# Kernel tuning notes

Hardware: AMD Instinct MI355X
Metric: run time of the kernel (lower is better)

The kernel has to match this reference:

```python
import jax, jax.numpy as jnp
import numpy as np

NUM_HEADS = 32


def setup_inputs() -> dict:
    key = jax.random.key(0)
    ks = jax.random.split(key, 6)
    B, S, D = 1, 2048, 4096
    hd = D // NUM_HEADS  # 128
    x = jax.random.normal(ks[0], (B, S, D), dtype=jnp.float32)
    # true rotary frequencies: freqs_cis = exp(i * t * theta^{-2j/hd})
    inv_freq = 1.0 / (10000.0 ** (jnp.arange(0, hd, 2, dtype=jnp.float32) / hd))  # [hd//2]
    angles = jnp.arange(S, dtype=jnp.float32)[:, None] * inv_freq[None, :]  # [S, hd//2]
    freqs_cos = jnp.cos(angles)
    freqs_sin = jnp.sin(angles)
    scale = 0.02
    wq = jax.random.normal(ks[1], (D, D), dtype=jnp.float32) * scale
    wk = jax.random.normal(ks[2], (D, D), dtype=jnp.float32) * scale
    wv = jax.random.normal(ks[3], (D, D), dtype=jnp.float32) * scale
    wo = jax.random.normal(ks[4], (D, D), dtype=jnp.float32) * scale
    return {"x": x, "freqs_cos": freqs_cos, "freqs_sin": freqs_sin,
            "wq": wq, "wk": wk, "wv": wv, "wo": wo}


def _apply_rope(t, cos, sin):
    # t: [B, S, H, hd]; cos/sin: [S, hd//2]
    B, S, H, hd = t.shape
    tr = t.reshape(B, S, H, hd // 2, 2)
    a, b = tr[..., 0], tr[..., 1]
    c = cos[None, :, None, :]
    s = sin[None, :, None, :]
    out_r = a * c - b * s
    out_i = a * s + b * c
    return jnp.stack([out_r, out_i], axis=-1).reshape(B, S, H, hd)


def reference(x, freqs_cos, freqs_sin, wq, wk, wv, wo):
    B, S, D = x.shape
    H = NUM_HEADS
    hd = D // H
    xq = (x @ wq).reshape(B, S, H, hd)
    xk = (x @ wk).reshape(B, S, H, hd)
    xv = (x @ wv).reshape(B, S, H, hd)
    xq = _apply_rope(xq, freqs_cos, freqs_sin)
    xk = _apply_rope(xk, freqs_cos, freqs_sin)
    # [B, H, S, hd]
    xq = xq.transpose(0, 2, 1, 3)
    xk = xk.transpose(0, 2, 1, 3)
    xv = xv.transpose(0, 2, 1, 3)
    scores = jnp.einsum('bhqd,bhkd->bhqk', xq, xk) / jnp.sqrt(jnp.float32(hd))
    scores = jax.nn.softmax(scores.astype(jnp.float32), axis=-1).astype(xq.dtype)
    out = jnp.einsum('bhqk,bhkd->bhqd', scores, xv)
    out = out.transpose(0, 2, 1, 3).reshape(B, S, D)
    return out @ wo
```

## Files before the change

### kernel.cpp

```cpp
#include <hip/hip_runtime.h>
#include <hip/hip_bf16.h>

typedef __hip_bfloat16 bf16;
typedef __attribute__((ext_vector_type(8))) short short8;
typedef __attribute__((ext_vector_type(4))) short short4v;
typedef __attribute__((ext_vector_type(4))) float f32x4;

#define MFMA16(a, b, c) __builtin_amdgcn_mfma_f32_16x16x32_bf16((a), (b), (c), 0, 0, 0)
#define EXP2(x) __builtin_amdgcn_exp2f(x)

static __device__ __forceinline__ void gload_lds16(const bf16* g, bf16* l) {
  __builtin_amdgcn_global_load_lds((const __attribute__((address_space(1))) unsigned int*)g,
                                   (__attribute__((address_space(3))) unsigned int*)l,
                                   16, 0, 0);
}

__global__ __launch_bounds__(256) void prepN_kernel(const float* __restrict__ x,
                                                    bf16* __restrict__ xb,
                                                    const float* __restrict__ wq,
                                                    const float* __restrict__ wk,
                                                    const float* __restrict__ wv,
                                                    const float* __restrict__ wo,
                                                    bf16* __restrict__ wT2,
                                                    bf16* __restrict__ wvT,
                                                    bf16* __restrict__ woT) {
  int y = blockIdx.y;
  if (y == 2) {
    int i = (blockIdx.x * 256 + threadIdx.x) * 8;
    float4 v0 = *(const float4*)(x + i);
    float4 v1 = *(const float4*)(x + i + 4);
    bf16 tmp[8];
    tmp[0] = __float2bfloat16(v0.x); tmp[1] = __float2bfloat16(v0.y);
    tmp[2] = __float2bfloat16(v0.z); tmp[3] = __float2bfloat16(v0.w);
    tmp[4] = __float2bfloat16(v1.x); tmp[5] = __float2bfloat16(v1.y);
    tmp[6] = __float2bfloat16(v1.z); tmp[7] = __float2bfloat16(v1.w);
    *(short8*)(xb + i) = *(short8*)tmp;
    return;
  }
  const float* W;
  bf16* WT;
  if (y == 0)      { W = wq; WT = wT2; }
  else if (y == 1) { W = wk; WT = wT2 + (size_t)4096 * 4096; }
  else if (y == 3) { W = wv; WT = wvT; }
  else             { W = wo; WT = woT; }
  __shared__ bf16 tile[64][65];
  int b = blockIdx.x;
  int tk = (b >> 6) * 64;
  int tn = (b & 63) * 64;
  int t = threadIdx.x;
  int c = t & 63, r0 = t >> 6;
#pragma unroll
  for (int i = 0; i < 16; ++i) {
    int r = i * 4 + r0;
    tile[c][r] = __float2bfloat16(W[(size_t)(tk + r) * 4096 + tn + c]);
  }
  __syncthreads();
#pragma unroll
  for (int i = 0; i < 16; ++i) {
    int r = i * 4 + r0;
    WT[(size_t)(tn + r) * 4096 + tk + c] = tile[r][c];
  }
}

__global__ __launch_bounds__(256) void tw_kernel(const float* __restrict__ W,
                                                 bf16* __restrict__ WT) {
  __shared__ bf16 tile[64][65];
  int b = blockIdx.x;
  int tk = (b >> 6) * 64;
  int tn = (b & 63) * 64;
  int t = threadIdx.x;
  int c = t & 63, r0 = t >> 6;
#pragma unroll
  for (int i = 0; i < 16; ++i) {
    int r = i * 4 + r0;
    tile[c][r] = __float2bfloat16(W[(size_t)(tk + r) * 4096 + tn + c]);
  }
  __syncthreads();
#pragma unroll
  for (int i = 0; i < 16; ++i) {
    int r = i * 4 + r0;
    WT[(size_t)(tn + r) * 4096 + tk + c] = tile[r][c];
  }
}

__global__ __launch_bounds__(512) void gemmQK8(const bf16* __restrict__ A,
                                               const bf16* __restrict__ Bt,
                                               bf16* __restrict__ Qb,
                                               bf16* __restrict__ Kb,
                                               const float* __restrict__ fcos,
                                               const float* __restrict__ fsin) {
  __shared__ bf16 LDS[2 * 32768];
  const int K = 4096, NK = 64;
  int g = blockIdx.x;
  int xcd = g & 7, loc = g >> 3;
  int bm = (xcd >> 2) * 4 + (loc >> 3);
  int bn = (xcd & 3) * 8 + (loc & 7);
  int t = threadIdx.x, lane = t & 63, w = t >> 6;
  int wm = w >> 2, wn = w & 3;
  int lr = lane & 15, lg = lane >> 4;
  int rsw = (lr >> 1) & 3;
  f32x4 acc[8][4] = {};

  const bf16* Ab = A + (size_t)bm * 256 * K;
  const bf16* Bb = Bt + (size_t)bn * 256 * K;
  int sr4 = t >> 2;
  int sg = (t & 3) ^ ((t >> 3) & 3);

#define SA(nb, kt2, kh)                                                          \
  do {                                                                           \
    _Pragma("unroll") for (int j = 0; j < 2; ++j)                                \
      gload_lds16(Ab + (size_t)(j * 128 + sr4) * K + (kt2) * 64 + (kh) * 32 + sg * 8, \
                  LDS + (nb) + (kh) * 8192 + (j * 512 + t) * 8);                 \
  } while (0)
#define SB(nb, kt2, kh)                                                          \
  do {                                                                           \
    _Pragma("unroll") for (int j = 0; j < 2; ++j)                                \
      gload_lds16(Bb + (size_t)(j * 128 + sr4) * K + (kt2) * 64 + (kh) * 32 + sg * 8, \
                  LDS + (nb) + 16384 + (kh) * 8192 + (j * 512 + t) * 8);         \
  } while (0)
#define AFR(base, kc, mi) \
  (*(const short8*)(LDS + (base) + (kc) * 8192 + (wm * 128 + (mi) * 16 + lr) * 32 + ((lg ^ rsw) << 3)))
#define BFR(base, kc, nf) \
  (*(const short8*)(LDS + (base) + 16384 + (kc) * 8192 + (wn * 64 + (nf) * 16 + lr) * 32 + ((lg ^ rsw) << 3)))

  SA(0, 0, 0); SB(0, 0, 0); SA(0, 0, 1); SB(0, 0, 1);
  asm volatile("s_waitcnt vmcnt(4)" ::: "memory");
  __builtin_amdgcn_s_barrier();

  int cur = 0;
  for (int kt = 0; kt < NK; ++kt) {
    int base = cur * 32768;
    int nbf = (cur ^ 1) * 32768;
    bool pf = (kt + 1) < NK;
    short8 a[4], b[4];

#pragma unroll
    for (int nf = 0; nf < 4; ++nf) b[nf] = BFR(base, 0, nf);
#pragma unroll
    for (int i = 0; i < 4; ++i) a[i] = AFR(base, 0, i);
    if (pf) SA(nbf, kt + 1, 0);
    __builtin_amdgcn_s_setprio(1);
#pragma unroll
    for (int i = 0; i < 4; ++i)
#pragma unroll
      for (int nf = 0; nf < 4; ++nf)
        acc[i][nf] = MFMA16(a[i], b[nf], acc[i][nf]);
    __builtin_amdgcn_s_setprio(0);
#pragma unroll
    for (int i = 0; i < 4; ++i) a[i] = AFR(base, 0, 4 + i);
    if (pf) SB(nbf, kt + 1, 0);
    __builtin_amdgcn_s_setprio(1);
#pragma unroll
    for (int i = 0; i < 4; ++i)
#pragma unroll
      for (int nf = 0; nf < 4; ++nf)
        acc[4 + i][nf] = MFMA16(a[i], b[nf], acc[4 + i][nf]);
    __builtin_amdgcn_s_setprio(0);
    if (pf)
      asm volatile("s_waitcnt vmcnt(4)" ::: "memory");
    else
      asm volatile("s_waitcnt vmcnt(0)" ::: "memory");
    __builtin_amdgcn_s_barrier();

#pragma unroll
    for (int nf = 0; nf < 4; ++nf) b[nf] = BFR(base, 1, nf);
#pragma unroll
    for (int i = 0; i < 4; ++i) a[i] = AFR(base, 1, i);
    if (pf) SA(nbf, kt + 1, 1);
    __builtin_amdgcn_s_setprio(1);
#pragma unroll
    for (int i = 0; i < 4; ++i)
#pragma unroll
      for (int nf = 0; nf < 4; ++nf)
        acc[i][nf] = MFMA16(a[i], b[nf], acc[i][nf]);
    __builtin_amdgcn_s_setprio(0);
#pragma unroll
    for (int i = 0; i < 4; ++i) a[i] = AFR(base, 1, 4 + i);
    if (pf) SB(nbf, kt + 1, 1);
    __builtin_amdgcn_s_setprio(1);
#pragma unroll
    for (int i = 0; i < 4; ++i)
#pragma unroll
      for (int nf = 0; nf < 4; ++nf)
        acc[4 + i][nf] = MFMA16(a[i], b[nf], acc[4 + i][nf]);
    __builtin_amdgcn_s_setprio(0);
    asm volatile("s_waitcnt vmcnt(4)" ::: "memory");
    __builtin_amdgcn_s_barrier();

    cur ^= 1;
  }
#undef SA
#undef SB
#undef AFR
#undef BFR

  int sect = bn >> 4, bnl = bn & 15;
  bf16* Cb = sect ? Kb : Qb;
  const float qs = sect ? 1.0f : (0.08838834764831845f * 1.4426950408889634f);
#pragma unroll
  for (int mi = 0; mi < 8; ++mi)
#pragma unroll
    for (int nf = 0; nf < 4; ++nf) {
      int col = bnl * 256 + wn * 64 + nf * 16 + lr;
      int row0 = bm * 256 + wm * 128 + mi * 16 + lg * 4;
      int ip = (col >> 1) & 63;
      float sgn = (col & 1) ? 1.0f : -1.0f;
#pragma unroll
      for (int r = 0; r < 4; ++r) {
        int row = row0 + r;
        float mine = acc[mi][nf][r];
        float oth = __shfl_xor(mine, 1);
        float cv = fcos[row * 64 + ip];
        float sv = fsin[row * 64 + ip];
        float v = (mine * cv + sgn * oth * sv) * qs;
        Cb[(size_t)row * 4096 + col] = __float2bfloat16(v);
      }
    }
}

template <int EPI>
__global__ __launch_bounds__(512) void gemmB3(const bf16* __restrict__ A,
                                              const bf16* __restrict__ Bt,
                                              void* __restrict__ Cv,
                                              int M, int N) {
  __shared__ bf16 LDS[2 * 24576];
  const int K = 4096, NK = 64;
  int g = blockIdx.x;
  int xcd = g & 7, loc = g >> 3;
  int bm = (xcd >> 1) * 4 + (loc >> 3);
  int bn = (xcd & 1) * 8 + (loc & 7);
  int t = threadIdx.x, lane = t & 63, w = t >> 6;
  int wm = w >> 2, wn = w & 3;
  int lr = lane & 15, lg = lane >> 4;
  int rsw = (lr >> 1) & 3;
  f32x4 acc[4][4] = {};

  const bf16* Ab = A + (size_t)bm * 128 * K;
  const bf16* Bb = Bt + (size_t)bn * 256 * K;
  int sr4 = t >> 2;
  int sg = (t & 3) ^ ((t >> 3) & 3);

#define SAB(nb, kt2, kh)                                                         \
  gload_lds16(Ab + (size_t)sr4 * K + (kt2) * 64 + (kh) * 32 + sg * 8,            \
              LDS + (nb) + (kh) * 4096 + t * 8)
#define SBB(nb, kt2, kh)                                                         \
  do {                                                                           \
    _Pragma("unroll") for (int j = 0; j < 2; ++j)                                \
      gload_lds16(Bb + (size_t)(j * 128 + sr4) * K + (kt2) * 64 + (kh) * 32 + sg * 8, \
                  LDS + (nb) + 8192 + (kh) * 8192 + (j * 512 + t) * 8);          \
  } while (0)
#define AFRB(base, kc, mi) \
  (*(const short8*)(LDS + (base) + (kc) * 4096 + ((wm * 64 + (mi) * 16 + lr) * 32) + ((lg ^ rsw) << 3)))
#define BFRB(base, kc, nf) \
  (*(const short8*)(LDS + (base) + 8192 + (kc) * 8192 + (wn * 64 + (nf) * 16 + lr) * 32 + ((lg ^ rsw) << 3)))

  SAB(0, 0, 0); SBB(0, 0, 0); SAB(0, 0, 1); SBB(0, 0, 1);
  asm volatile("s_waitcnt vmcnt(3)" ::: "memory");
  __builtin_amdgcn_s_barrier();

  int cur = 0;
  for (int kt = 0; kt < NK; ++kt) {
    int base = cur * 24576;
    int nbf = (cur ^ 1) * 24576;
    bool pf = (kt + 1) < NK;
    short8 a[4], b[4];

#pragma unroll
    for (int nf = 0; nf < 4; ++nf) b[nf] = BFRB(base, 0, nf);
#pragma unroll
    for (int i = 0; i < 4; ++i) a[i] = AFRB(base, 0, i);
    if (pf) { SAB(nbf, kt + 1, 0); SBB(nbf, kt + 1, 0); }
    __builtin_amdgcn_s_setprio(1);
#pragma unroll
    for (int i = 0; i < 4; ++i)
#pragma unroll
      for (int nf = 0; nf < 4; ++nf)
        acc[i][nf] = MFMA16(a[i], b[nf], acc[i][nf]);
    __builtin_amdgcn_s_setprio(0);
    if (pf)
      asm volatile("s_waitcnt vmcnt(3)" ::: "memory");
    else
      asm volatile("s_waitcnt vmcnt(0)" ::: "memory");
    __builtin_amdgcn_s_barrier();

#pragma unroll
    for (int nf = 0; nf < 4; ++nf) b[nf] = BFRB(base, 1, nf);
#pragma unroll
    for (int i = 0; i < 4; ++i) a[i] = AFRB(base, 1, i);
    if (pf) { SAB(nbf, kt + 1, 1); SBB(nbf, kt + 1, 1); }
    __builtin_amdgcn_s_setprio(1);
#pragma unroll
    for (int i = 0; i < 4; ++i)
#pragma unroll
      for (int nf = 0; nf < 4; ++nf)
        acc[i][nf] = MFMA16(a[i], b[nf], acc[i][nf]);
    __builtin_amdgcn_s_setprio(0);
    asm volatile("s_waitcnt vmcnt(3)" ::: "memory");
    __builtin_amdgcn_s_barrier();

    cur ^= 1;
  }
#undef SAB
#undef SBB
#undef AFRB
#undef BFRB

#pragma unroll
  for (int mi = 0; mi < 4; ++mi)
#pragma unroll
    for (int nf = 0; nf < 4; ++nf) {
      int col = bn * 256 + wn * 64 + nf * 16 + lr;
      int row0 = bm * 128 + wm * 64 + mi * 16 + lg * 4;
      if constexpr (EPI == 3) {
        bf16 tmp[4];
#pragma unroll
        for (int r = 0; r < 4; ++r) tmp[r] = __float2bfloat16(acc[mi][nf][r]);
        *(short4v*)((bf16*)Cv + (size_t)col * M + row0) = *(short4v*)tmp;
      } else {
#pragma unroll
        for (int r = 0; r < 4; ++r)
          ((float*)Cv)[(size_t)(row0 + r) * N + col] = acc[mi][nf][r];
      }
    }
}

__global__ __launch_bounds__(512, 2) void attn_fwd(const bf16* __restrict__ Q,
                                                   const bf16* __restrict__ K,
                                                   const bf16* __restrict__ Vt,
                                                   bf16* __restrict__ O) {
  __shared__ bf16 Kbuf[2][64 * 128];
  __shared__ bf16 Vbuf[2][128 * 64];
  __shared__ char Ps_all[8][2][2048];
  const int S = 2048, D = 4096, HD = 128, NT = 32;
  int g = blockIdx.y * 8 + blockIdx.x;
  int wid = (g & 7) * 32 + (g >> 3);
  int h = wid >> 3, qb = wid & 7;
  int tid = threadIdx.x, lane = tid & 63, w = tid >> 6;
  int lr = lane & 15, lg = lane >> 4;
  int q0 = qb * 256 + w * 32;
  int swz = (lr & 7) << 4;

  const bf16* Kh = K + h * HD;
  const bf16* Vh = Vt + (size_t)h * HD * S;

  short8 aq[2][4];
#pragma unroll
  for (int u = 0; u < 2; ++u)
#pragma unroll
    for (int c = 0; c < 4; ++c)
      aq[u][c] = *(const short8*)(Q + (size_t)(q0 + u * 16 + lr) * D + h * HD + c * 32 + lg * 8);

  int kr = lane >> 4, ksl = lane & 15;
  int vr = lane >> 3, vsl = lane & 7;

  f32x4 accO[2][8] = {};
  float lsum[2] = {0.f, 0.f};

#define STAGE(b, ttile)                                                            \
  do {                                                                             \
    int kv0_ = (ttile) * 64;                                                       \
    _Pragma("unroll") for (int ii = 0; ii < 2; ++ii) {                             \
      int row = w * 8 + ii * 4 + kr;                                               \
      gload_lds16(Kh + (size_t)(kv0_ + row) * D + ((ksl ^ (row & 7)) << 3),        \
                  &Kbuf[b][(w * 8 + ii * 4) * 128]);                               \
    }                                                                              \
    _Pragma("unroll") for (int ii = 0; ii < 2; ++ii) {                             \
      int row = w * 16 + ii * 8 + vr;                                              \
      gload_lds16(Vh + (size_t)row * S + kv0_ + ((vsl ^ (row & 7)) << 3),          \
                  &Vbuf[b][(w * 16 + ii * 8) * 64]);                               \
    }                                                                              \
  } while (0)

  int cur = 0;
  STAGE(0, 0);
  for (int tt = 0; tt < NT; ++tt) {
    if (tt + 1 < NT) {
      STAGE(cur ^ 1, tt + 1);
      asm volatile("s_waitcnt vmcnt(4)" ::: "memory");
    } else {
      asm volatile("s_waitcnt vmcnt(0)" ::: "memory");
    }
    __builtin_amdgcn_s_barrier();
    const bf16* Kb_ = Kbuf[cur];
    const bf16* Vb_ = Vbuf[cur];

    f32x4 sf[2][4] = {};
    __builtin_amdgcn_s_setprio(1);
#pragma unroll
    for (int j = 0; j < 4; ++j)
#pragma unroll
      for (int c = 0; c < 4; ++c) {
        short8 kf = *(const short8*)(Kb_ + (j * 16 + lr) * 128 +
                                     (((c * 4 + lg) ^ (lr & 7)) << 3));
        sf[0][j] = MFMA16(kf, aq[0][c], sf[0][j]);
        sf[1][j] = MFMA16(kf, aq[1][c], sf[1][j]);
      }
    __builtin_amdgcn_s_setprio(0);
#pragma unroll
    for (int u = 0; u < 2; ++u) {
      char* Ps = Ps_all[w][u];
#pragma unroll
      for (int j = 0; j < 4; ++j) {
        float p0 = EXP2(sf[u][j][0]);
        float p1 = EXP2(sf[u][j][1]);
        float p2 = EXP2(sf[u][j][2]);
        float p3 = EXP2(sf[u][j][3]);
        lsum[u] += (p0 + p1) + (p2 + p3);
        bf16 pk[4] = {__float2bfloat16(p0), __float2bfloat16(p1),
                      __float2bfloat16(p2), __float2bfloat16(p3)};
        *(short4v*)(Ps + lr * 128 + ((j * 32 + lg * 8) ^ swz)) = *(short4v*)pk;
      }
    }
#pragma unroll
    for (int t2 = 0; t2 < 2; ++t2) {
      short8 pa0 = *(const short8*)(Ps_all[w][0] + lr * 128 + ((t2 * 64 + lg * 16) ^ swz));
      short8 pa1 = *(const short8*)(Ps_all[w][1] + lr * 128 + ((t2 * 64 + lg * 16) ^ swz));
      __builtin_amdgcn_s_setprio(1);
#pragma unroll
      for (int n = 0; n < 8; ++n) {
        short8 bv = *(const short8*)(Vb_ + (n * 16 + lr) * 64 +
                                     (((t2 * 4 + lg) ^ (lr & 7)) << 3));
        accO[0][n] = MFMA16(pa0, bv, accO[0][n]);
        accO[1][n] = MFMA16(pa1, bv, accO[1][n]);
      }
      __builtin_amdgcn_s_setprio(0);
    }
    __builtin_amdgcn_s_barrier();
    cur ^= 1;
  }
#undef STAGE

#pragma unroll
  for (int u = 0; u < 2; ++u) {
    float ls = lsum[u];
    ls += __shfl_xor(ls, 16);
    ls += __shfl_xor(ls, 32);
    float rs[4];
#pragma unroll
    for (int r = 0; r < 4; ++r)
      rs[r] = 1.f / __shfl(ls, lg * 4 + r);
#pragma unroll
    for (int n = 0; n < 8; ++n)
#pragma unroll
      for (int r = 0; r < 4; ++r) {
        int row = q0 + u * 16 + lg * 4 + r;
        int col = h * HD + n * 16 + lr;
        O[(size_t)row * D + col] = __float2bfloat16(accO[u][n][r] * rs[r]);
      }
  }
}

extern "C" void kernel_launch(void* const* d_in, const int* in_sizes, int n_in,
                              void* d_out, int out_size, void* d_ws, size_t ws_size,
                              hipStream_t stream) {
  const float* x    = (const float*)d_in[0];
  const float* fcos = (const float*)d_in[1];
  const float* fsin = (const float*)d_in[2];
  const float* wq   = (const float*)d_in[3];
  const float* wk   = (const float*)d_in[4];
  const float* wv   = (const float*)d_in[5];
  const float* wo   = (const float*)d_in[6];
  float* out = (float*)d_out;

  const int S = 2048, D = 4096;
  const size_t MB = 1024 * 1024;
  char* ws = (char*)d_ws;
  bf16* xb  = (bf16*)(ws);
  bf16* wT2 = (bf16*)(ws + 16 * MB);
  bf16* Vt  = (bf16*)(ws + 48 * MB);
  bf16* Qb  = (bf16*)(ws + 80 * MB);
  bf16* Kb  = (bf16*)(ws + 96 * MB);
  bf16* wvT = (bf16*)(ws + 112 * MB);
  bf16* woT = (bf16*)(ws + 144 * MB);
  bf16* AO  = (bf16*)(ws);

  bool haveV = ws_size >= 144 * MB;
  bool haveO = ws_size >= 176 * MB;
  int ny = 3 + (haveV ? 1 : 0) + (haveO ? 1 : 0);

  prepN_kernel<<<dim3(4096, ny), 256, 0, stream>>>(x, xb, wq, wk, wv, wo, wT2, wvT, woT);
  gemmQK8<<<256, 512, 0, stream>>>(xb, wT2, Qb, Kb, fcos, fsin);

  if (!haveV) tw_kernel<<<4096, 256, 0, stream>>>(wv, wT2);
  gemmB3<3><<<256, 512, 0, stream>>>(xb, haveV ? wvT : wT2, Vt, S, D);

  attn_fwd<<<dim3(8, 32), 512, 0, stream>>>(Qb, Kb, Vt, AO);

  if (!haveO) tw_kernel<<<4096, 256, 0, stream>>>(wo, wT2);
  gemmB3<4><<<256, 512, 0, stream>>>(AO, haveO ? woT : wT2, out, S, D);
}
```

Before: 400.1 us.

## Retile QK projection GEMM to 256x128 tiles with triple-buffered K=32 pipeline

Changes the fused Q/K projection GEMM from 256x256 tiles with K-step 64 and double buffering to 256x128 tiles with K-step 32 and a three-stage LDS ring, prefetching two steps ahead. The grid doubles to 512 blocks and LDS use shrinks, so more blocks fill the CUs and occupancy can rise. In exchange each block reuses less operand data (lower arithmetic intensity per tile), and there are twice as many barrier iterations per K.

```diff
diff --git a/kernel.cpp b/kernel.cpp
--- a/kernel.cpp
+++ b/kernel.cpp
@@ -83,62 +83,60 @@
   }
 }
 
-__global__ __launch_bounds__(512) void gemmQK8(const bf16* __restrict__ A,
-                                               const bf16* __restrict__ Bt,
-                                               bf16* __restrict__ Qb,
-                                               bf16* __restrict__ Kb,
-                                               const float* __restrict__ fcos,
-                                               const float* __restrict__ fsin) {
-  __shared__ bf16 LDS[2 * 32768];
-  const int K = 4096, NK = 64;
+__global__ __launch_bounds__(512) void gemmQK32(const bf16* __restrict__ A,
+                                                const bf16* __restrict__ Bt,
+                                                bf16* __restrict__ Qb,
+                                                bf16* __restrict__ Kb,
+                                                const float* __restrict__ fcos,
+                                                const float* __restrict__ fsin) {
+  __shared__ bf16 LDS[3 * 12288];
+  const int K = 4096, NK = 128;
   int g = blockIdx.x;
   int xcd = g & 7, loc = g >> 3;
-  int bm = (xcd >> 2) * 4 + (loc >> 3);
-  int bn = (xcd & 3) * 8 + (loc & 7);
+  int bm = (xcd >> 2) * 4 + (loc >> 4);
+  int bn = (xcd & 3) * 16 + (loc & 15);
   int t = threadIdx.x, lane = t & 63, w = t >> 6;
-  int wm = w >> 2, wn = w & 3;
+  int wm = w >> 1, wn = w & 1;
   int lr = lane & 15, lg = lane >> 4;
   int rsw = (lr >> 1) & 3;
-  f32x4 acc[8][4] = {};
+  f32x4 acc[4][4] = {};
 
   const bf16* Ab = A + (size_t)bm * 256 * K;
-  const bf16* Bb = Bt + (size_t)bn * 256 * K;
+  const bf16* Bb = Bt + (size_t)bn * 128 * K;
   int sr4 = t >> 2;
   int sg = (t & 3) ^ ((t >> 3) & 3);
 
-#define SA(nb, kt2, kh)                                                          \
+#define SA32(buf, kt2)                                                           \
   do {                                                                           \
     _Pragma("unroll") for (int j = 0; j < 2; ++j)                                \
-      gload_lds16(Ab + (size_t)(j * 128 + sr4) * K + (kt2) * 64 + (kh) * 32 + sg * 8, \
-                  LDS + (nb) + (kh) * 8192 + (j * 512 + t) * 8);                 \
+      gload_lds16(Ab + (size_t)(j * 128 + sr4) * K + (kt2) * 32 + sg * 8,        \
+                  LDS + (buf) * 12288 + (j * 512 + t) * 8);                      \
   } while (0)
-#define SB(nb, kt2, kh)                                                          \
-  do {                                                                           \
-    _Pragma("unroll") for (int j = 0; j < 2; ++j)                                \
-      gload_lds16(Bb + (size_t)(j * 128 + sr4) * K + (kt2) * 64 + (kh) * 32 + sg * 8, \
-                  LDS + (nb) + 16384 + (kh) * 8192 + (j * 512 + t) * 8);         \
-  } while (0)
-#define AFR(base, kc, mi) \
-  (*(const short8*)(LDS + (base) + (kc) * 8192 + (wm * 128 + (mi) * 16 + lr) * 32 + ((lg ^ rsw) << 3)))
-#define BFR(base, kc, nf) \
-  (*(const short8*)(LDS + (base) + 16384 + (kc) * 8192 + (wn * 64 + (nf) * 16 + lr) * 32 + ((lg ^ rsw) << 3)))
-
-  SA(0, 0, 0); SB(0, 0, 0); SA(0, 0, 1); SB(0, 0, 1);
-  asm volatile("s_waitcnt vmcnt(4)" ::: "memory");
+#define SB32(buf, kt2)                                                           \
+  gload_lds16(Bb + (size_t)sr4 * K + (kt2) * 32 + sg * 8,                        \
+              LDS + (buf) * 12288 + 8192 + t * 8)
+#define AFR32(base, mi) \
+  (*(const short8*)(LDS + (base) + (wm * 64 + (mi) * 16 + lr) * 32 + ((lg ^ rsw) << 3)))
+#define BFR32(base, nf) \
+  (*(const short8*)(LDS + (base) + 8192 + (wn * 64 + (nf) * 16 + lr) * 32 + ((lg ^ rsw) << 3)))
+
+  SA32(0, 0); SB32(0, 0);
+  SA32(1, 1); SB32(1, 1);
+  asm volatile("s_waitcnt vmcnt(3)" ::: "memory");
   __builtin_amdgcn_s_barrier();
 
   int cur = 0;
   for (int kt = 0; kt < NK; ++kt) {
-    int base = cur * 32768;
-    int nbf = (cur ^ 1) * 32768;
-    bool pf = (kt + 1) < NK;
+    int base = cur * 12288;
+    int sb = cur + 2; if (sb >= 3) sb -= 3;
+    bool pf = (kt + 2) < NK;
     short8 a[4], b[4];
 
 #pragma unroll
-    for (int nf = 0; nf < 4; ++nf) b[nf] = BFR(base, 0, nf);
-#pragma unroll
-    for (int i = 0; i < 4; ++i) a[i] = AFR(base, 0, i);
-    if (pf) SA(nbf, kt + 1, 0);
+    for (int nf = 0; nf < 4; ++nf) b[nf] = BFR32(base, nf);
+#pragma unroll
+    for (int i = 0; i < 4; ++i) a[i] = AFR32(base, i);
+    if (pf) { SA32(sb, kt + 2); SB32(sb, kt + 2); }
     __builtin_amdgcn_s_setprio(1);
 #pragma unroll
     for (int i = 0; i < 4; ++i)
@@ -146,63 +144,28 @@
       for (int nf = 0; nf < 4; ++nf)
         acc[i][nf] = MFMA16(a[i], b[nf], acc[i][nf]);
     __builtin_amdgcn_s_setprio(0);
-#pragma unroll
-    for (int i = 0; i < 4; ++i) a[i] = AFR(base, 0, 4 + i);
-    if (pf) SB(nbf, kt + 1, 0);
-    __builtin_amdgcn_s_setprio(1);
-#pragma unroll
-    for (int i = 0; i < 4; ++i)
-#pragma unroll
-      for (int nf = 0; nf < 4; ++nf)
-        acc[4 + i][nf] = MFMA16(a[i], b[nf], acc[4 + i][nf]);
-    __builtin_amdgcn_s_setprio(0);
     if (pf)
-      asm volatile("s_waitcnt vmcnt(4)" ::: "memory");
+      asm volatile("s_waitcnt vmcnt(3)" ::: "memory");
     else
       asm volatile("s_waitcnt vmcnt(0)" ::: "memory");
     __builtin_amdgcn_s_barrier();
 
-#pragma unroll
-    for (int nf = 0; nf < 4; ++nf) b[nf] = BFR(base, 1, nf);
-#pragma unroll
-    for (int i = 0; i < 4; ++i) a[i] = AFR(base, 1, i);
-    if (pf) SA(nbf, kt + 1, 1);
-    __builtin_amdgcn_s_setprio(1);
-#pragma unroll
-    for (int i = 0; i < 4; ++i)
-#pragma unroll
-      for (int nf = 0; nf < 4; ++nf)
-        acc[i][nf] = MFMA16(a[i], b[nf], acc[i][nf]);
-    __builtin_amdgcn_s_setprio(0);
-#pragma unroll
-    for (int i = 0; i < 4; ++i) a[i] = AFR(base, 1, 4 + i);
-    if (pf) SB(nbf, kt + 1, 1);
-    __builtin_amdgcn_s_setprio(1);
-#pragma unroll
-    for (int i = 0; i < 4; ++i)
-#pragma unroll
-      for (int nf = 0; nf < 4; ++nf)
-        acc[4 + i][nf] = MFMA16(a[i], b[nf], acc[4 + i][nf]);
-    __builtin_amdgcn_s_setprio(0);
-    asm volatile("s_waitcnt vmcnt(4)" ::: "memory");
-    __builtin_amdgcn_s_barrier();
-
-    cur ^= 1;
-  }
-#undef SA
-#undef SB
-#undef AFR
-#undef BFR
-
-  int sect = bn >> 4, bnl = bn & 15;
+    cur = (cur + 1 == 3) ? 0 : cur + 1;
+  }
+#undef SA32
+#undef SB32
+#undef AFR32
+#undef BFR32
+
+  int sect = bn >> 5, bnl = bn & 31;
   bf16* Cb = sect ? Kb : Qb;
   const float qs = sect ? 1.0f : (0.08838834764831845f * 1.4426950408889634f);
 #pragma unroll
-  for (int mi = 0; mi < 8; ++mi)
+  for (int mi = 0; mi < 4; ++mi)
 #pragma unroll
     for (int nf = 0; nf < 4; ++nf) {
-      int col = bnl * 256 + wn * 64 + nf * 16 + lr;
-      int row0 = bm * 256 + wm * 128 + mi * 16 + lg * 4;
+      int col = bnl * 128 + wn * 64 + nf * 16 + lr;
+      int row0 = bm * 256 + wm * 64 + mi * 16 + lg * 4;
       int ip = (col >> 1) & 63;
       float sgn = (col & 1) ? 1.0f : -1.0f;
 #pragma unroll
@@ -479,7 +442,7 @@
   int ny = 3 + (haveV ? 1 : 0) + (haveO ? 1 : 0);
 
   prepN_kernel<<<dim3(4096, ny), 256, 0, stream>>>(x, xb, wq, wk, wv, wo, wT2, wvT, woT);
-  gemmQK8<<<256, 512, 0, stream>>>(xb, wT2, Qb, Kb, fcos, fsin);
+  gemmQK32<<<512, 512, 0, stream>>>(xb, wT2, Qb, Kb, fcos, fsin);
 
   if (!haveV) tw_kernel<<<4096, 256, 0, stream>>>(wv, wT2);
   gemmB3<3><<<256, 512, 0, stream>>>(xb, haveV ? wvT : wT2, Vt, S, D);
```

Measured after the change: 424.8 us. +6.2%, slower.
